# Performance work log

Hardware: AMD Instinct MI355X
Metric: run time of the kernel (lower is better)

## Reference

```python
import jax, jax.numpy as jnp
import numpy as np

N_NODES = 50000
N_EDGES = 800000
IN_C, HID_C, OUT_C = 128, 128, 64


def setup_inputs() -> dict:
    key = jax.random.key(0)
    ks = jax.random.split(key, 8)
    x = jax.random.normal(ks[0], (N_NODES, IN_C), dtype=jnp.float32)
    edge_index = jax.random.randint(ks[1], (2, N_EDGES), 0, N_NODES, dtype=jnp.int64)
    def glorot(k, shape):
        lim = np.sqrt(6.0 / (shape[0] + shape[1])).astype(np.float32)
        return jax.random.uniform(k, shape, jnp.float32, -lim, lim)
    return {
        "x": x,
        "edge_index": edge_index,
        "W1l": glorot(ks[2], (IN_C, HID_C)),
        "b1": jnp.zeros((HID_C,), jnp.float32),
        "W1r": glorot(ks[3], (IN_C, HID_C)),
        "W2l": glorot(ks[4], (HID_C, OUT_C)),
        "b2": jnp.zeros((OUT_C,), jnp.float32),
        "W2r": glorot(ks[5], (HID_C, OUT_C)),
    }


def _sage_conv(h, src, dst, Wl, bl, Wr):
    # mean aggregation over incoming edges (source -> target)
    n = h.shape[0]
    msg_sum = jax.ops.segment_sum(h[src], dst, num_segments=n)          # [N, d]
    deg = jax.ops.segment_sum(jnp.ones((src.shape[0],), h.dtype), dst, num_segments=n)
    agg = msg_sum / jnp.maximum(deg, 1.0)[:, None]                      # zero-degree -> 0
    # lin_l(agg) + lin_r(h); lin_l carries the bias (PyG SAGEConv default)
    return agg @ Wl + bl + h @ Wr


def reference(x, edge_index, W1l, b1, W1r, W2l, b2, W2r):
    src, dst = edge_index[0], edge_index[1]
    h = jax.nn.relu(_sage_conv(x, src, dst, W1l, b1, W1r))
    # eval-mode forward: dropout is identity
    out = _sage_conv(h, src, dst, W2l, b2, W2r)
    return out
```

## Files before the change

### kernel.cpp

```cpp
#include <hip/hip_runtime.h>

#define N_NODES 50000
#define N_EDGES 800000
#define IN_C    128
#define HID_C   128
#define OUT_C   64
#define NBIN    1563
#define BCAP8   768
#define QCAP8   768
#define EPB     2048
#define EBLKS   ((N_EDGES + EPB - 1) / EPB)
#define PACK_BLKS 192
#define MM1_BLKS  ((N_NODES + 63) / 64)
#define HS_STRIDE 136

typedef unsigned short ushort_t;
typedef unsigned int   uint_t;
typedef unsigned char  uchar_t;
typedef __attribute__((ext_vector_type(8))) short bf16x8;
typedef __attribute__((ext_vector_type(4))) float f32x4;
typedef __attribute__((ext_vector_type(2))) float f32x2;

__device__ inline ushort_t f2bf(float f) {
    uint_t u = __float_as_uint(f);
    uint_t r = (u + 0x7fffu + ((u >> 16) & 1u)) >> 16;
    return (ushort_t)r;
}
__device__ inline float bflo(uint_t v) { return __uint_as_float(v << 16); }
__device__ inline float bfhi(uint_t v) { return __uint_as_float(v & 0xffff0000u); }
__device__ inline uchar_t f2fp8(float v) {
    return (uchar_t)(__builtin_amdgcn_cvt_pk_fp8_f32(v, v, 0, false) & 0xff);
}
__device__ inline void acc_fp8x4(float* a, uint_t d) {
    const f32x2 lo = __builtin_amdgcn_cvt_pk_f32_fp8((int)d, false);
    const f32x2 hi = __builtin_amdgcn_cvt_pk_f32_fp8((int)d, true);
    a[0] += lo.x; a[1] += lo.y; a[2] += hi.x; a[3] += hi.y;
}
__device__ inline void acc_uint4(float* a, const uint4 v) {
    acc_fp8x4(a + 0,  v.x);
    acc_fp8x4(a + 4,  v.y);
    acc_fp8x4(a + 8,  v.z);
    acc_fp8x4(a + 12, v.w);
}

__device__ inline void pack_one(const float* W, ushort_t* Wp, int K, int N, int idx) {
    const int j  = idx & 7;
    const int L  = (idx >> 3) & 63;
    const int t  = idx >> 9;
    const int KT = K / 32;
    const int kt = t % KT;
    const int ct = t / KT;
    const int k  = kt * 32 + (L >> 4) * 8 + j;
    const int n  = ct * 16 + (L & 15);
    Wp[idx] = f2bf(W[k * N + n]);
}

__global__ __launch_bounds__(256) void k0_kernel(
    const float* __restrict__ W1l, const float* __restrict__ W1r,
    const float* __restrict__ W2l, const float* __restrict__ W2r,
    ushort_t* __restrict__ wpack, int* __restrict__ gcur)
{
    const int b = blockIdx.x;
    if (b < PACK_BLKS) {
        const int tid = b * 256 + threadIdx.x;
        if (tid < 16384)      pack_one(W1l, wpack,          IN_C,  HID_C, tid);
        else if (tid < 32768) pack_one(W1r, wpack + 16384,  IN_C,  HID_C, tid - 16384);
        else if (tid < 40960) pack_one(W2l, wpack + 32768,  HID_C, OUT_C, tid - 32768);
        else if (tid < 49152) pack_one(W2r, wpack + 40960,  HID_C, OUT_C, tid - 40960);
    } else {
        for (int i = threadIdx.x; i < NBIN; i += 256) gcur[i] = 0;
    }
}

__device__ inline void mm1_body(int bid, const float* __restrict__ x,
                                const ushort_t* __restrict__ wpack,
                                uchar_t* __restrict__ p1f, ushort_t* __restrict__ t1b)
{
    const int wave = threadIdx.x >> 6;
    const int lane = threadIdx.x & 63;
    const int quad = lane >> 4;
    const int m    = lane & 15;
    const int row0 = bid * 64 + wave * 16;
    const int arow = min(row0 + m, N_NODES - 1);

    const bf16x8* Bl = (const bf16x8*)(wpack);
    const bf16x8* Br = (const bf16x8*)(wpack + 16384);

    f32x4 accl[8], accr[8];
#pragma unroll
    for (int ct = 0; ct < 8; ++ct) { accl[ct] = (f32x4)(0.0f); accr[ct] = (f32x4)(0.0f); }

    const float* xbase = x + (size_t)arow * IN_C + quad * 8;
    float4 c0 = *(const float4*)(xbase);
    float4 c1 = *(const float4*)(xbase + 4);

#pragma unroll
    for (int kt = 0; kt < 4; ++kt) {
        float4 n0 = c0, n1 = c1;
        if (kt < 3) {
            n0 = *(const float4*)(xbase + (kt + 1) * 32);
            n1 = *(const float4*)(xbase + (kt + 1) * 32 + 4);
        }
        bf16x8 af;
        af[0] = (short)f2bf(c0.x); af[1] = (short)f2bf(c0.y);
        af[2] = (short)f2bf(c0.z); af[3] = (short)f2bf(c0.w);
        af[4] = (short)f2bf(c1.x); af[5] = (short)f2bf(c1.y);
        af[6] = (short)f2bf(c1.z); af[7] = (short)f2bf(c1.w);
#pragma unroll
        for (int ct = 0; ct < 8; ++ct) {
            const bf16x8 bl = Bl[(ct * 4 + kt) * 64 + lane];
            const bf16x8 br = Br[(ct * 4 + kt) * 64 + lane];
            accl[ct] = __builtin_amdgcn_mfma_f32_16x16x32_bf16(af, bl, accl[ct], 0, 0, 0);
            accr[ct] = __builtin_amdgcn_mfma_f32_16x16x32_bf16(af, br, accr[ct], 0, 0, 0);
        }
        c0 = n0; c1 = n1;
    }

#pragma unroll
    for (int r = 0; r < 4; ++r) {
        const int orow = row0 + quad * 4 + r;
        if (orow < N_NODES) {
#pragma unroll
            for (int ct = 0; ct < 8; ++ct) {
                const int col = ct * 16 + m;
                p1f[(size_t)orow * HID_C + col] = f2fp8(accl[ct][r]);
                t1b[(size_t)orow * HID_C + col] = f2bf(accr[ct][r]);
            }
        }
    }
}

__global__ __launch_bounds__(256) void k1_kernel(
    const float* __restrict__ x, const ushort_t* __restrict__ wpack,
    uchar_t* __restrict__ p1f, ushort_t* __restrict__ t1b,
    const int* __restrict__ src, const int* __restrict__ dst,
    int* gcur, int* __restrict__ ebuf)
{
    __shared__ int lh[NBIN], gb2[NBIN], lc[NBIN];
    const int b = blockIdx.x;
    if (b < MM1_BLKS) {
        mm1_body(b, x, wpack, p1f, t1b);
        return;
    }
    const int blk = b - MM1_BLKS;
    const int t = threadIdx.x;
    for (int i = t; i < NBIN; i += 256) lh[i] = 0;
    __syncthreads();
    const int e0 = blk * EPB + t * 8;
    int v8[8], b8[8];
    if (e0 < N_EDGES) {
        const int4 sa = *(const int4*)&src[e0];
        const int4 sb = *(const int4*)&src[e0 + 4];
        const int4 da = *(const int4*)&dst[e0];
        const int4 db = *(const int4*)&dst[e0 + 4];
        const int s8a[8] = {sa.x, sa.y, sa.z, sa.w, sb.x, sb.y, sb.z, sb.w};
        const int d8a[8] = {da.x, da.y, da.z, da.w, db.x, db.y, db.z, db.w};
#pragma unroll
        for (int j = 0; j < 8; ++j) {
            b8[j] = d8a[j] >> 5;
            v8[j] = (s8a[j] << 5) | (d8a[j] & 31);
            atomicAdd(&lh[b8[j]], 1);
        }
    } else {
#pragma unroll
        for (int j = 0; j < 8; ++j) b8[j] = -1;
    }
    __syncthreads();
    for (int i = t; i < NBIN; i += 256) {
        const int run = lh[i];
        gb2[i] = (run > 0) ? atomicAdd(&gcur[i], run) : 0;
        lc[i] = 0;
    }
    __syncthreads();
#pragma unroll
    for (int j = 0; j < 8; ++j) {
        const int bk = b8[j];
        if (bk >= 0) {
            const int p   = atomicAdd(&lc[bk], 1);
            const int pos = gb2[bk] + p;
            if (pos < BCAP8) ebuf[bk * BCAP8 + pos] = v8[j];
        }
    }
}

__global__ __launch_bounds__(256, 4) void l2f_kernel(
    const int* __restrict__ ebuf, const int* __restrict__ gcur,
    int* __restrict__ cnt, int* __restrict__ row_ptr, int* __restrict__ csr_g,
    const uchar_t* __restrict__ p1f, const ushort_t* __restrict__ t1b,
    const float* __restrict__ b1,
    const ushort_t* __restrict__ wpack,
    uchar_t* __restrict__ p2f, ushort_t* __restrict__ t2b)
{
    __shared__ ushort_t hs[32 * HS_STRIDE];
    __shared__ __align__(16) int csr_lds[QCAP8];
    __shared__ int lh[32], lstart[32], lcur2[32];
    __shared__ int pool, ltotal;

    const int blk = blockIdx.x;
    const int tid = threadIdx.x;

    if (tid == 0) pool = 0;
    if (tid < 32) lh[tid] = 0;
    __syncthreads();

    const int nb   = min(gcur[blk], BCAP8);
    const int base = blk * BCAP8;
    int v0 = -1, v1 = -1, v2 = -1;
    if (tid       < nb) v0 = ebuf[base + tid];
    if (tid + 256 < nb) v1 = ebuf[base + tid + 256];
    if (tid + 512 < nb) v2 = ebuf[base + tid + 512];
    if (v0 >= 0) atomicAdd(&lh[v0 & 31], 1);
    if (v1 >= 0) atomicAdd(&lh[v1 & 31], 1);
    if (v2 >= 0) atomicAdd(&lh[v2 & 31], 1);
    __syncthreads();
    if (tid < 32) {
        const int c = lh[tid];
        int v = c;
#pragma unroll
        for (int off = 1; off < 32; off <<= 1) {
            const int u = __shfl_up(v, off, 32);
            if (tid >= off) v += u;
        }
        const int ex = v - c;
        lstart[tid] = ex;
        lcur2[tid]  = ex;
        if (tid == 31) ltotal = v;
        const int node = blk * 32 + tid;
        if (node < N_NODES) { cnt[node] = c; row_ptr[node] = blk * QCAP8 + ex; }
    }
    __syncthreads();
    if (v0 >= 0) { const int p = atomicAdd(&lcur2[v0 & 31], 1); if (p < QCAP8) csr_lds[p] = v0 >> 5; }
    if (v1 >= 0) { const int p = atomicAdd(&lcur2[v1 & 31], 1); if (p < QCAP8) csr_lds[p] = v1 >> 5; }
    if (v2 >= 0) { const int p = atomicAdd(&lcur2[v2 & 31], 1); if (p < QCAP8) csr_lds[p] = v2 >> 5; }
    __syncthreads();
    {
        const int total = ltotal > QCAP8 ? QCAP8 : ltotal;
        const int nt4 = (total + 3) >> 2;
        int4* dst4 = (int4*)(csr_g + blk * QCAP8);
        const int4* src4 = (const int4*)csr_lds;
        for (int i = tid; i < nt4; i += 256) dst4[i] = src4[i];
    }
    __syncthreads();

    const int c16 = tid & 7;
    const int gb  = (tid & 63) & 56;
    const uint4* p1v = (const uint4*)p1f;

    while (true) {
        int nl = 0;
        if (c16 == 0) nl = atomicAdd(&pool, 1);
        nl = __shfl(nl, gb, 64);
        if (nl >= 32) break;
        const int node = blk * 32 + nl;
        uint4 oL = make_uint4(0u, 0u, 0u, 0u);
        uint4 oH = make_uint4(0u, 0u, 0u, 0u);
        if (node < N_NODES) {
            const int start = lstart[nl];
            const int degi  = lh[nl];
            const size_t ib = (size_t)node * HID_C + c16 * 16;
            const uint4 tvL = *(const uint4*)(t1b + ib);
            const uint4 tvH = *(const uint4*)(t1b + ib + 8);
            float a[16];
#pragma unroll
            for (int z = 0; z < 16; ++z) a[z] = 0.0f;
            int e = 0;
            for (; e + 3 < degi; e += 4) {
                const int s0 = csr_lds[start + e + 0];
                const int s1 = csr_lds[start + e + 1];
                const int s2 = csr_lds[start + e + 2];
                const int s3 = csr_lds[start + e + 3];
                const uint4 w0 = p1v[(size_t)s0 * 8 + c16];
                const uint4 w1 = p1v[(size_t)s1 * 8 + c16];
                const uint4 w2 = p1v[(size_t)s2 * 8 + c16];
                const uint4 w3 = p1v[(size_t)s3 * 8 + c16];
                acc_uint4(a, w0); acc_uint4(a, w1); acc_uint4(a, w2); acc_uint4(a, w3);
            }
            for (; e < degi; ++e) {
                const uint4 v = p1v[(size_t)csr_lds[start + e] * 8 + c16];
                acc_uint4(a, v);
            }
            const float inv = 1.0f / fmaxf((float)degi, 1.0f);
            float r[16];
#pragma unroll
            for (int z = 0; z < 4; ++z) {
                const float4 bv = *(const float4*)(b1 + c16 * 16 + z * 4);
                r[z*4+0] = bv.x; r[z*4+1] = bv.y; r[z*4+2] = bv.z; r[z*4+3] = bv.w;
            }
            const uint_t tw[8] = {tvL.x, tvL.y, tvL.z, tvL.w, tvH.x, tvH.y, tvH.z, tvH.w};
#pragma unroll
            for (int z = 0; z < 8; ++z) {
                r[z*2+0] = fmaxf(fmaf(a[z*2+0], inv, r[z*2+0] + bflo(tw[z])), 0.0f);
                r[z*2+1] = fmaxf(fmaf(a[z*2+1], inv, r[z*2+1] + bfhi(tw[z])), 0.0f);
            }
            oL.x = (uint_t)f2bf(r[0])  | ((uint_t)f2bf(r[1])  << 16);
            oL.y = (uint_t)f2bf(r[2])  | ((uint_t)f2bf(r[3])  << 16);
            oL.z = (uint_t)f2bf(r[4])  | ((uint_t)f2bf(r[5])  << 16);
            oL.w = (uint_t)f2bf(r[6])  | ((uint_t)f2bf(r[7])  << 16);
            oH.x = (uint_t)f2bf(r[8])  | ((uint_t)f2bf(r[9])  << 16);
            oH.y = (uint_t)f2bf(r[10]) | ((uint_t)f2bf(r[11]) << 16);
            oH.z = (uint_t)f2bf(r[12]) | ((uint_t)f2bf(r[13]) << 16);
            oH.w = (uint_t)f2bf(r[14]) | ((uint_t)f2bf(r[15]) << 16);
        }
        *(uint4*)&hs[nl * HS_STRIDE + c16 * 16] = oL;
        *(uint4*)&hs[nl * HS_STRIDE + c16 * 16 + 8] = oH;
    }
    __syncthreads();

    const int wv    = tid >> 6;
    const int lane  = tid & 63;
    const int quad  = lane >> 4;
    const int m     = lane & 15;
    const int rhalf = wv & 1;
    const int chalf = (wv >> 1) * 2;
    const int row0  = blk * 32 + rhalf * 16;

    const bf16x8* Bl = (const bf16x8*)(wpack + 32768);
    const bf16x8* Br = (const bf16x8*)(wpack + 40960);

    f32x4 accl[2], accr[2];
#pragma unroll
    for (int c2 = 0; c2 < 2; ++c2) { accl[c2] = (f32x4)(0.0f); accr[c2] = (f32x4)(0.0f); }

#pragma unroll
    for (int kt = 0; kt < 4; ++kt) {
        const bf16x8 af = *(const bf16x8*)&hs[(rhalf * 16 + m) * HS_STRIDE + kt * 32 + quad * 8];
#pragma unroll
        for (int c2 = 0; c2 < 2; ++c2) {
            const int ct = chalf + c2;
            const bf16x8 bl = Bl[(ct * 4 + kt) * 64 + lane];
            const bf16x8 br = Br[(ct * 4 + kt) * 64 + lane];
            accl[c2] = __builtin_amdgcn_mfma_f32_16x16x32_bf16(af, bl, accl[c2], 0, 0, 0);
            accr[c2] = __builtin_amdgcn_mfma_f32_16x16x32_bf16(af, br, accr[c2], 0, 0, 0);
        }
    }

#pragma unroll
    for (int r = 0; r < 4; ++r) {
        const int orow = row0 + quad * 4 + r;
        if (orow < N_NODES) {
#pragma unroll
            for (int c2 = 0; c2 < 2; ++c2) {
                const int col = (chalf + c2) * 16 + m;
                p2f[(size_t)orow * OUT_C + col] = f2fp8(accl[c2][r]);
                t2b[(size_t)orow * OUT_C + col] = f2bf(accr[c2][r]);
            }
        }
    }
}

__global__ __launch_bounds__(256) void agg2_kernel(
    const uchar_t* __restrict__ p2f, const ushort_t* __restrict__ t2b,
    const float* __restrict__ b2, const int* __restrict__ row_ptr,
    const int* __restrict__ cnt, const int* __restrict__ csr,
    float* __restrict__ out)
{
    const int c16 = threadIdx.x & 3;
    const int grp = threadIdx.x >> 2;
    const uint4* p2v = (const uint4*)p2f;

    const int node = blockIdx.x * 64 + grp;
    if (node >= N_NODES) return;
    const int start = row_ptr[node];
    const int degi  = cnt[node];
    const size_t i = (size_t)node * OUT_C + c16 * 16;
    const uint4 tvL = *(const uint4*)(t2b + i);
    const uint4 tvH = *(const uint4*)(t2b + i + 8);
    float a[16];
#pragma unroll
    for (int z = 0; z < 16; ++z) a[z] = 0.0f;
    int e = 0;
    for (; e + 3 < degi; e += 4) {
        const int s0 = csr[start + e + 0];
        const int s1 = csr[start + e + 1];
        const int s2 = csr[start + e + 2];
        const int s3 = csr[start + e + 3];
        const uint4 w0 = p2v[(size_t)s0 * 4 + c16];
        const uint4 w1 = p2v[(size_t)s1 * 4 + c16];
        const uint4 w2 = p2v[(size_t)s2 * 4 + c16];
        const uint4 w3 = p2v[(size_t)s3 * 4 + c16];
        acc_uint4(a, w0); acc_uint4(a, w1); acc_uint4(a, w2); acc_uint4(a, w3);
    }
    for (; e < degi; ++e) {
        const uint4 v = p2v[(size_t)csr[start + e] * 4 + c16];
        acc_uint4(a, v);
    }

    const float inv = 1.0f / fmaxf((float)degi, 1.0f);
    const uint_t tw[8] = {tvL.x, tvL.y, tvL.z, tvL.w, tvH.x, tvH.y, tvH.z, tvH.w};
#pragma unroll
    for (int z = 0; z < 4; ++z) {
        const float4 bv = *(const float4*)(b2 + c16 * 16 + z * 4);
        float4 o;
        o.x = fmaf(a[z*4+0], inv, bv.x + bflo(tw[z*2+0]));
        o.y = fmaf(a[z*4+1], inv, bv.y + bfhi(tw[z*2+0]));
        o.z = fmaf(a[z*4+2], inv, bv.z + bflo(tw[z*2+1]));
        o.w = fmaf(a[z*4+3], inv, bv.w + bfhi(tw[z*2+1]));
        *(float4*)(out + i + z * 4) = o;
    }
}

extern "C" void kernel_launch(void* const* d_in, const int* in_sizes, int n_in,
                              void* d_out, int out_size, void* d_ws, size_t ws_size,
                              hipStream_t stream)
{
    const float* x   = (const float*)d_in[0];
    const int*   ei  = (const int*)d_in[1];
    const float* W1l = (const float*)d_in[2];
    const float* b1  = (const float*)d_in[3];
    const float* W1r = (const float*)d_in[4];
    const float* W2l = (const float*)d_in[5];
    const float* b2  = (const float*)d_in[6];
    const float* W2r = (const float*)d_in[7];
    float* out = (float*)d_out;

    const int* src = ei;
    const int* dst = ei + N_EDGES;

    const size_t NH = (size_t)N_NODES * HID_C;
    const size_t NO = (size_t)N_NODES * OUT_C;
    const size_t EB = (size_t)NBIN * BCAP8;
    const size_t CB = (size_t)NBIN * QCAP8;

    char* ws = (char*)d_ws;
    ushort_t* t1b   = (ushort_t*)ws;                   ws += NH * sizeof(ushort_t);
    ushort_t* t2b   = (ushort_t*)ws;                   ws += NO * sizeof(ushort_t);
    ushort_t* wpack = (ushort_t*)ws;                   ws += 49152 * sizeof(ushort_t);
    int* ebuf    = (int*)ws;                           ws += EB * sizeof(int);
    int* csr     = (int*)ws;                           ws += CB * sizeof(int);
    int* cnt     = (int*)ws;                           ws += N_NODES * sizeof(int);
    int* row_ptr = (int*)ws;                           ws += N_NODES * sizeof(int);
    int* gcur    = (int*)ws;                           ws += NBIN * sizeof(int);
    ws += (16 - ((size_t)(ws - (char*)d_ws) & 15)) & 15;
    uchar_t* p1f = (uchar_t*)ws;                       ws += NH * sizeof(uchar_t);
    uchar_t* p2f = (uchar_t*)ws;                       ws += NO * sizeof(uchar_t);

    const size_t need = (size_t)(ws - (char*)d_ws);
    if (ws_size < need) return;

    k0_kernel<<<PACK_BLKS + 1, 256, 0, stream>>>(W1l, W1r, W2l, W2r, wpack, gcur);
    k1_kernel<<<MM1_BLKS + EBLKS, 256, 0, stream>>>(
        x, wpack, p1f, t1b, src, dst, gcur, ebuf);
    l2f_kernel<<<NBIN, 256, 0, stream>>>(
        ebuf, gcur, cnt, row_ptr, csr, p1f, t1b, b1, wpack, p2f, t2b);
    agg2_kernel<<<MM1_BLKS, 256, 0, stream>>>(
        p2f, t2b, b2, row_ptr, cnt, csr, out);
}
```

Before: 157.8 us.

## Fuse all stages into one cooperative persistent kernel with grid syncs

Replaces the four separate launches (weight pack, scatter+mm1, l2f, agg2) with a single cooperative kernel of 512 persistent blocks. The stages are separated by grid.sync, and each stage takes its work units from an atomic counter queue. The queue counters sit right after gcur and are zeroed together with it. This removes launch gaps and inter-kernel drain, but in exchange it runs fewer resident blocks, so there is less latency hiding for the gather-heavy phases. It also adds grid-barrier cost and makes the register budget the maximum across all stage bodies. If the cooperative launch fails, it falls back to the old multi-kernel path.

New measurement: 173.0 us. +9.6%, slower.

```diff
diff --git a/kernel.cpp b/kernel.cpp
--- a/kernel.cpp
+++ b/kernel.cpp
@@ -1,4 +1,7 @@
 #include <hip/hip_runtime.h>
+#include <hip/hip_cooperative_groups.h>
+
+namespace cg = cooperative_groups;
 
 #define N_NODES 50000
 #define N_EDGES 800000
@@ -13,6 +16,8 @@
 #define PACK_BLKS 192
 #define MM1_BLKS  ((N_NODES + 63) / 64)
 #define HS_STRIDE 136
+#define SMEM_BYTES (3 * NBIN * 4)
+#define COOP_BLOCKS 512
 
 typedef unsigned short ushort_t;
 typedef unsigned int   uint_t;
@@ -55,21 +60,17 @@
     Wp[idx] = f2bf(W[k * N + n]);
 }
 
-__global__ __launch_bounds__(256) void k0_kernel(
-    const float* __restrict__ W1l, const float* __restrict__ W1r,
-    const float* __restrict__ W2l, const float* __restrict__ W2r,
-    ushort_t* __restrict__ wpack, int* __restrict__ gcur)
-{
-    const int b = blockIdx.x;
-    if (b < PACK_BLKS) {
-        const int tid = b * 256 + threadIdx.x;
-        if (tid < 16384)      pack_one(W1l, wpack,          IN_C,  HID_C, tid);
-        else if (tid < 32768) pack_one(W1r, wpack + 16384,  IN_C,  HID_C, tid - 16384);
-        else if (tid < 40960) pack_one(W2l, wpack + 32768,  HID_C, OUT_C, tid - 32768);
-        else if (tid < 49152) pack_one(W2r, wpack + 40960,  HID_C, OUT_C, tid - 40960);
-    } else {
-        for (int i = threadIdx.x; i < NBIN; i += 256) gcur[i] = 0;
-    }
+__device__ inline void pack_body(int vb, const float* __restrict__ W1l,
+                                 const float* __restrict__ W1r,
+                                 const float* __restrict__ W2l,
+                                 const float* __restrict__ W2r,
+                                 ushort_t* __restrict__ wpack)
+{
+    const int tid = vb * 256 + threadIdx.x;
+    if (tid < 16384)      pack_one(W1l, wpack,          IN_C,  HID_C, tid);
+    else if (tid < 32768) pack_one(W1r, wpack + 16384,  IN_C,  HID_C, tid - 16384);
+    else if (tid < 40960) pack_one(W2l, wpack + 32768,  HID_C, OUT_C, tid - 32768);
+    else if (tid < 49152) pack_one(W2r, wpack + 40960,  HID_C, OUT_C, tid - 40960);
 }
 
 __device__ inline void mm1_body(int bid, const float* __restrict__ x,
@@ -130,19 +131,13 @@
     }
 }
 
-__global__ __launch_bounds__(256) void k1_kernel(
-    const float* __restrict__ x, const ushort_t* __restrict__ wpack,
-    uchar_t* __restrict__ p1f, ushort_t* __restrict__ t1b,
-    const int* __restrict__ src, const int* __restrict__ dst,
-    int* gcur, int* __restrict__ ebuf)
-{
-    __shared__ int lh[NBIN], gb2[NBIN], lc[NBIN];
-    const int b = blockIdx.x;
-    if (b < MM1_BLKS) {
-        mm1_body(b, x, wpack, p1f, t1b);
-        return;
-    }
-    const int blk = b - MM1_BLKS;
+__device__ inline void scatter_body(int blk, const int* __restrict__ src,
+                                    const int* __restrict__ dst,
+                                    int* gcur, int* __restrict__ ebuf, char* smem)
+{
+    int* lh  = (int*)smem;
+    int* gb2 = lh + NBIN;
+    int* lc  = gb2 + NBIN;
     const int t = threadIdx.x;
     for (int i = t; i < NBIN; i += 256) lh[i] = 0;
     __syncthreads();
@@ -183,23 +178,23 @@
     }
 }
 
-__global__ __launch_bounds__(256, 4) void l2f_kernel(
+__device__ inline void l2f_body(int blk,
     const int* __restrict__ ebuf, const int* __restrict__ gcur,
     int* __restrict__ cnt, int* __restrict__ row_ptr, int* __restrict__ csr_g,
     const uchar_t* __restrict__ p1f, const ushort_t* __restrict__ t1b,
-    const float* __restrict__ b1,
-    const ushort_t* __restrict__ wpack,
-    uchar_t* __restrict__ p2f, ushort_t* __restrict__ t2b)
-{
-    __shared__ ushort_t hs[32 * HS_STRIDE];
-    __shared__ __align__(16) int csr_lds[QCAP8];
-    __shared__ int lh[32], lstart[32], lcur2[32];
-    __shared__ int pool, ltotal;
-
-    const int blk = blockIdx.x;
+    const float* __restrict__ b1, const ushort_t* __restrict__ wpack,
+    uchar_t* __restrict__ p2f, ushort_t* __restrict__ t2b, char* smem)
+{
+    ushort_t* hs     = (ushort_t*)smem;
+    int* csr_lds     = (int*)(smem + 8704);
+    int* lh          = (int*)(smem + 11776);
+    int* lstart      = (int*)(smem + 11904);
+    int* lcur2       = (int*)(smem + 12032);
+    int* pool        = (int*)(smem + 12160);
+    int* ltotal      = (int*)(smem + 12164);
+
     const int tid = threadIdx.x;
-
-    if (tid == 0) pool = 0;
+    if (tid == 0) *pool = 0;
     if (tid < 32) lh[tid] = 0;
     __syncthreads();
 
@@ -224,7 +219,7 @@
         const int ex = v - c;
         lstart[tid] = ex;
         lcur2[tid]  = ex;
-        if (tid == 31) ltotal = v;
+        if (tid == 31) *ltotal = v;
         const int node = blk * 32 + tid;
         if (node < N_NODES) { cnt[node] = c; row_ptr[node] = blk * QCAP8 + ex; }
     }
@@ -234,7 +229,7 @@
     if (v2 >= 0) { const int p = atomicAdd(&lcur2[v2 & 31], 1); if (p < QCAP8) csr_lds[p] = v2 >> 5; }
     __syncthreads();
     {
-        const int total = ltotal > QCAP8 ? QCAP8 : ltotal;
+        const int total = *ltotal > QCAP8 ? QCAP8 : *ltotal;
         const int nt4 = (total + 3) >> 2;
         int4* dst4 = (int4*)(csr_g + blk * QCAP8);
         const int4* src4 = (const int4*)csr_lds;
@@ -248,7 +243,7 @@
 
     while (true) {
         int nl = 0;
-        if (c16 == 0) nl = atomicAdd(&pool, 1);
+        if (c16 == 0) nl = atomicAdd(pool, 1);
         nl = __shfl(nl, gb, 64);
         if (nl >= 32) break;
         const int node = blk * 32 + nl;
@@ -348,55 +343,149 @@
     }
 }
 
+__device__ inline void agg2_body(int vb,
+    const uchar_t* __restrict__ p2f, const ushort_t* __restrict__ t2b,
+    const float* __restrict__ b2, const int* __restrict__ row_ptr,
+    const int* __restrict__ cnt, const int* __restrict__ csr,
+    float* __restrict__ out)
+{
+    const int c16 = threadIdx.x & 3;
+    const int grp = threadIdx.x >> 2;
+    const uint4* p2v = (const uint4*)p2f;
+
+    const int node = vb * 64 + grp;
+    if (node < N_NODES) {
+        const int start = row_ptr[node];
+        const int degi  = cnt[node];
+        const size_t i = (size_t)node * OUT_C + c16 * 16;
+        const uint4 tvL = *(const uint4*)(t2b + i);
+        const uint4 tvH = *(const uint4*)(t2b + i + 8);
+        float a[16];
+#pragma unroll
+        for (int z = 0; z < 16; ++z) a[z] = 0.0f;
+        int e = 0;
+        for (; e + 3 < degi; e += 4) {
+            const int s0 = csr[start + e + 0];
+            const int s1 = csr[start + e + 1];
+            const int s2 = csr[start + e + 2];
+            const int s3 = csr[start + e + 3];
+            const uint4 w0 = p2v[(size_t)s0 * 4 + c16];
+            const uint4 w1 = p2v[(size_t)s1 * 4 + c16];
+            const uint4 w2 = p2v[(size_t)s2 * 4 + c16];
+            const uint4 w3 = p2v[(size_t)s3 * 4 + c16];
+            acc_uint4(a, w0); acc_uint4(a, w1); acc_uint4(a, w2); acc_uint4(a, w3);
+        }
+        for (; e < degi; ++e) {
+            const uint4 v = p2v[(size_t)csr[start + e] * 4 + c16];
+            acc_uint4(a, v);
+        }
+        const float inv = 1.0f / fmaxf((float)degi, 1.0f);
+        const uint_t tw[8] = {tvL.x, tvL.y, tvL.z, tvL.w, tvH.x, tvH.y, tvH.z, tvH.w};
+#pragma unroll
+        for (int z = 0; z < 4; ++z) {
+            const float4 bv = *(const float4*)(b2 + c16 * 16 + z * 4);
+            float4 o;
+            o.x = fmaf(a[z*4+0], inv, bv.x + bflo(tw[z*2+0]));
+            o.y = fmaf(a[z*4+1], inv, bv.y + bfhi(tw[z*2+0]));
+            o.z = fmaf(a[z*4+2], inv, bv.z + bflo(tw[z*2+1]));
+            o.w = fmaf(a[z*4+3], inv, bv.w + bfhi(tw[z*2+1]));
+            *(float4*)(out + i + z * 4) = o;
+        }
+    }
+}
+
+__global__ __launch_bounds__(256) void fused_kernel(
+    const float* __restrict__ x, const int* __restrict__ src, const int* __restrict__ dst,
+    const float* __restrict__ W1l, const float* __restrict__ b1, const float* __restrict__ W1r,
+    const float* __restrict__ W2l, const float* __restrict__ b2, const float* __restrict__ W2r,
+    ushort_t* wpack, int* gcur, int* qctr, int* ebuf, int* csr,
+    int* cnt, int* row_ptr, uchar_t* p1f, ushort_t* t1b,
+    uchar_t* p2f, ushort_t* t2b, float* out)
+{
+    __shared__ __align__(16) char smem[SMEM_BYTES];
+    __shared__ int unit_s;
+    cg::grid_group grid = cg::this_grid();
+
+    {
+        const int gtid = blockIdx.x * 256 + threadIdx.x;
+        const int gsz  = gridDim.x * 256;
+        for (int i = gtid; i < NBIN + 4; i += gsz) gcur[i] = 0;
+        for (int vb = blockIdx.x; vb < PACK_BLKS; vb += gridDim.x)
+            pack_body(vb, W1l, W1r, W2l, W2r, wpack);
+    }
+    grid.sync();
+
+    while (true) {
+        if (threadIdx.x == 0) unit_s = atomicAdd(&qctr[0], 1);
+        __syncthreads();
+        const int u = unit_s;
+        __syncthreads();
+        if (u >= EBLKS + MM1_BLKS) break;
+        if (u < EBLKS) scatter_body(u, src, dst, gcur, ebuf, smem);
+        else           mm1_body(u - EBLKS, x, wpack, p1f, t1b);
+    }
+    grid.sync();
+
+    while (true) {
+        if (threadIdx.x == 0) unit_s = atomicAdd(&qctr[1], 1);
+        __syncthreads();
+        const int u = unit_s;
+        __syncthreads();
+        if (u >= NBIN) break;
+        l2f_body(u, ebuf, gcur, cnt, row_ptr, csr, p1f, t1b, b1, wpack, p2f, t2b, smem);
+    }
+    grid.sync();
+
+    while (true) {
+        if (threadIdx.x == 0) unit_s = atomicAdd(&qctr[2], 1);
+        __syncthreads();
+        const int u = unit_s;
+        __syncthreads();
+        if (u >= MM1_BLKS) break;
+        agg2_body(u, p2f, t2b, b2, row_ptr, cnt, csr, out);
+    }
+}
+
+__global__ __launch_bounds__(256) void k0_kernel(
+    const float* __restrict__ W1l, const float* __restrict__ W1r,
+    const float* __restrict__ W2l, const float* __restrict__ W2r,
+    ushort_t* __restrict__ wpack, int* __restrict__ gcur)
+{
+    const int b = blockIdx.x;
+    if (b < PACK_BLKS) pack_body(b, W1l, W1r, W2l, W2r, wpack);
+    else { for (int i = threadIdx.x; i < NBIN; i += 256) gcur[i] = 0; }
+}
+
+__global__ __launch_bounds__(256) void k1_kernel(
+    const float* __restrict__ x, const ushort_t* __restrict__ wpack,
+    uchar_t* __restrict__ p1f, ushort_t* __restrict__ t1b,
+    const int* __restrict__ src, const int* __restrict__ dst,
+    int* gcur, int* __restrict__ ebuf)
+{
+    __shared__ __align__(16) char smem[SMEM_BYTES];
+    const int b = blockIdx.x;
+    if (b < MM1_BLKS) mm1_body(b, x, wpack, p1f, t1b);
+    else              scatter_body(b - MM1_BLKS, src, dst, gcur, ebuf, smem);
+}
+
+__global__ __launch_bounds__(256, 4) void l2f_kernel(
+    const int* __restrict__ ebuf, const int* __restrict__ gcur,
+    int* __restrict__ cnt, int* __restrict__ row_ptr, int* __restrict__ csr_g,
+    const uchar_t* __restrict__ p1f, const ushort_t* __restrict__ t1b,
+    const float* __restrict__ b1, const ushort_t* __restrict__ wpack,
+    uchar_t* __restrict__ p2f, ushort_t* __restrict__ t2b)
+{
+    __shared__ __align__(16) char smem[12176];
+    l2f_body(blockIdx.x, ebuf, gcur, cnt, row_ptr, csr_g, p1f, t1b, b1, wpack, p2f, t2b, smem);
+}
+
 __global__ __launch_bounds__(256) void agg2_kernel(
     const uchar_t* __restrict__ p2f, const ushort_t* __restrict__ t2b,
     const float* __restrict__ b2, const int* __restrict__ row_ptr,
     const int* __restrict__ cnt, const int* __restrict__ csr,
     float* __restrict__ out)
 {
-    const int c16 = threadIdx.x & 3;
-    const int grp = threadIdx.x >> 2;
-    const uint4* p2v = (const uint4*)p2f;
-
-    const int node = blockIdx.x * 64 + grp;
-    if (node >= N_NODES) return;
-    const int start = row_ptr[node];
-    const int degi  = cnt[node];
-    const size_t i = (size_t)node * OUT_C + c16 * 16;
-    const uint4 tvL = *(const uint4*)(t2b + i);
-    const uint4 tvH = *(const uint4*)(t2b + i + 8);
-    float a[16];
-#pragma unroll
-    for (int z = 0; z < 16; ++z) a[z] = 0.0f;
-    int e = 0;
-    for (; e + 3 < degi; e += 4) {
-        const int s0 = csr[start + e + 0];
-        const int s1 = csr[start + e + 1];
-        const int s2 = csr[start + e + 2];
-        const int s3 = csr[start + e + 3];
-        const uint4 w0 = p2v[(size_t)s0 * 4 + c16];
-        const uint4 w1 = p2v[(size_t)s1 * 4 + c16];
-        const uint4 w2 = p2v[(size_t)s2 * 4 + c16];
-        const uint4 w3 = p2v[(size_t)s3 * 4 + c16];
-        acc_uint4(a, w0); acc_uint4(a, w1); acc_uint4(a, w2); acc_uint4(a, w3);
-    }
-    for (; e < degi; ++e) {
-        const uint4 v = p2v[(size_t)csr[start + e] * 4 + c16];
-        acc_uint4(a, v);
-    }
-
-    const float inv = 1.0f / fmaxf((float)degi, 1.0f);
-    const uint_t tw[8] = {tvL.x, tvL.y, tvL.z, tvL.w, tvH.x, tvH.y, tvH.z, tvH.w};
-#pragma unroll
-    for (int z = 0; z < 4; ++z) {
-        const float4 bv = *(const float4*)(b2 + c16 * 16 + z * 4);
-        float4 o;
-        o.x = fmaf(a[z*4+0], inv, bv.x + bflo(tw[z*2+0]));
-        o.y = fmaf(a[z*4+1], inv, bv.y + bfhi(tw[z*2+0]));
-        o.z = fmaf(a[z*4+2], inv, bv.z + bflo(tw[z*2+1]));
-        o.w = fmaf(a[z*4+3], inv, bv.w + bfhi(tw[z*2+1]));
-        *(float4*)(out + i + z * 4) = o;
-    }
+    agg2_body(blockIdx.x, p2f, t2b, b2, row_ptr, cnt, csr, out);
 }
 
 extern "C" void kernel_launch(void* const* d_in, const int* in_sizes, int n_in,
@@ -430,12 +519,30 @@
     int* cnt     = (int*)ws;                           ws += N_NODES * sizeof(int);
     int* row_ptr = (int*)ws;                           ws += N_NODES * sizeof(int);
     int* gcur    = (int*)ws;                           ws += NBIN * sizeof(int);
+    int* qctr    = (int*)ws;                           ws += 4 * sizeof(int);
     ws += (16 - ((size_t)(ws - (char*)d_ws) & 15)) & 15;
     uchar_t* p1f = (uchar_t*)ws;                       ws += NH * sizeof(uchar_t);
     uchar_t* p2f = (uchar_t*)ws;                       ws += NO * sizeof(uchar_t);
 
     const size_t need = (size_t)(ws - (char*)d_ws);
     if (ws_size < need) return;
+
+    static int s_mode = 0;
+
+    if (s_mode >= 0) {
+        void* args[] = {
+            (void*)&x, (void*)&src, (void*)&dst,
+            (void*)&W1l, (void*)&b1, (void*)&W1r,
+            (void*)&W2l, (void*)&b2, (void*)&W2r,
+            (void*)&wpack, (void*)&gcur, (void*)&qctr, (void*)&ebuf, (void*)&csr,
+            (void*)&cnt, (void*)&row_ptr, (void*)&p1f, (void*)&t1b,
+            (void*)&p2f, (void*)&t2b, (void*)&out
+        };
+        hipError_t e = hipLaunchCooperativeKernel(fused_kernel, dim3(COOP_BLOCKS), dim3(256),
+                                                  args, 0u, stream);
+        if (e == hipSuccess) { s_mode = 1; return; }
+        s_mode = -1;
+    }
 
     k0_kernel<<<PACK_BLKS + 1, 256, 0, stream>>>(W1l, W1r, W2l, W2r, wpack, gcur);
     k1_kernel<<<MM1_BLKS + EBLKS, 256, 0, stream>>>(
```
